# Kernel optimization log

Hardware: AMD Instinct MI355X
Metric: run time of the kernel (lower is better)

## Reference

```python
import jax, jax.numpy as jnp
import numpy as np

N_NODES, N_EDGES = 50000, 800000
IN, HID, HEADS, OUT = 128, 64, 4, 64


def _segment_softmax(e, seg, n):
    # softmax over edges grouped by source node (torch.sparse.softmax dim=1), per head
    m = jax.ops.segment_max(e, seg, num_segments=n)
    ex = jnp.exp(e - m[seg])
    s = jax.ops.segment_sum(ex, seg, num_segments=n)
    return ex / s[seg]


def _attention_layer(x, src, dst, lw, lb, aw, ab, final):
    n = x.shape[0]
    h = jax.nn.leaky_relu(x @ lw.T + lb, 0.2)            # (N, F)
    f = h.shape[1]
    # Faithful decomposition of Conv1d(2*F*H, H, k=1, groups=H) applied to
    # concat([tile(h_i, H), tile(h_j, H)]): group k covers tiled copies 2k and 2k+1;
    # copies < H come from h_i (src), copies >= H from h_j (dst).
    k = jnp.arange(HEADS)
    sel1 = (2 * k < HEADS).astype(h.dtype)[:, None]       # first half of group weights
    sel2 = (2 * k + 1 < HEADS).astype(h.dtype)[:, None]   # second half
    Wi = aw[:, :f] * sel1 + aw[:, f:] * sel2              # (H, F) acting on h_src
    Wj = aw[:, :f] * (1.0 - sel1) + aw[:, f:] * (1.0 - sel2)  # (H, F) acting on h_dst
    e = (h @ Wi.T)[src] + (h @ Wj.T)[dst] + ab            # (E, H)
    alpha = _segment_softmax(e, src, n)                   # (E, H)
    # h2[i] = sum_{j in N(i)} h[j] outer alpha[ij]  -> (N, F, H)
    h2 = jax.ops.segment_sum(h[dst][:, :, None] * alpha[:, None, :], src, num_segments=n)
    if final:
        return jax.nn.relu(h2.mean(axis=-1))              # (N, OUT)
    return jax.nn.relu(h2.reshape(n, -1))                 # (N, F*H)


def setup_inputs() -> dict:
    key = jax.random.key(0)
    ks = jax.random.split(key, 16)
    d = {}
    d["x"] = jax.random.normal(ks[0], (N_NODES, IN), jnp.float32)
    dims_in = [IN, HID * HEADS, HID * HEADS]
    dims_out = [HID, HID, OUT]
    i = 1
    for L in range(3):
        di, do = dims_in[L], dims_out[L]
        d[f"lin{L}_w"] = jax.random.normal(ks[i], (do, di), jnp.float32) / np.float32(np.sqrt(di)); i += 1
        d[f"lin{L}_b"] = jax.random.normal(ks[i], (do,), jnp.float32) * 0.01; i += 1
        d[f"att{L}_w"] = jax.random.normal(ks[i], (HEADS, 2 * do), jnp.float32) / np.float32(np.sqrt(2 * do)); i += 1
        d[f"att{L}_b"] = jax.random.normal(ks[i], (HEADS,), jnp.float32) * 0.01; i += 1
    d["src"] = jnp.sort(jax.random.randint(ks[13], (N_EDGES,), 0, N_NODES, dtype=jnp.int32))
    d["dst"] = jax.random.randint(ks[14], (N_EDGES,), 0, N_NODES, dtype=jnp.int32)
    return d


def reference(x, lin0_w, lin0_b, att0_w, att0_b, lin1_w, lin1_b, att1_w, att1_b,
              lin2_w, lin2_b, att2_w, att2_b, src, dst):
    layers = [(lin0_w, lin0_b, att0_w, att0_b),
              (lin1_w, lin1_b, att1_w, att1_b),
              (lin2_w, lin2_b, att2_w, att2_b)]
    out = x
    for i, (lw, lb, aw, ab) in enumerate(layers):
        out = _attention_layer(out, src, dst, lw, lb, aw, ab, final=(i == len(layers) - 1))
    return out
```

## Files before the change

kernel.cpp:

```cpp
#include <hip/hip_runtime.h>
#include <hip/hip_fp16.h>

#define N_NODES 50000
#define N_EDGES 800000
#define BUCKET_SPLIT 25000

typedef _Float16 half8 __attribute__((ext_vector_type(8)));
typedef _Float16 f16x4 __attribute__((ext_vector_type(4)));
typedef float floatx4 __attribute__((ext_vector_type(4)));

__global__ __launch_bounds__(256) void setup_kernel(const int* __restrict__ src,
                                                    const int* __restrict__ dst,
                                                    int* __restrict__ row_ptr,
                                                    int* __restrict__ row_mid,
                                                    int* __restrict__ dstp,
                                                    const float* __restrict__ lw0,
                                                    const float* __restrict__ lw1,
                                                    const float* __restrict__ lw2,
                                                    _Float16* __restrict__ w0p,
                                                    _Float16* __restrict__ w1p,
                                                    _Float16* __restrict__ w2p) {
    const int gid = blockIdx.x * 256 + threadIdx.x;
    const int gstride = gridDim.x * 256;
    for (int idx = gid; idx <= N_NODES; idx += gstride) {
        int lo = 0, hi = N_EDGES;
        while (lo < hi) {
            int mid = (lo + hi) >> 1;
            if (src[mid] < idx) lo = mid + 1; else hi = mid;
        }
        row_ptr[idx] = lo;
    }
    for (int i = gid; i < N_NODES; i += gstride) {
        int lo = 0, hi = N_EDGES;
        while (lo < hi) { int m = (lo + hi) >> 1; if (src[m] < i) lo = m + 1; else hi = m; }
        int lo1 = lo, hi1 = N_EDGES;
        while (lo1 < hi1) { int m = (lo1 + hi1) >> 1; if (src[m] < i + 1) lo1 = m + 1; else hi1 = m; }
        int c = lo;
        for (int e = lo; e < lo1; ++e) { int d = dst[e]; if (d < BUCKET_SPLIT) dstp[c++] = d; }
        row_mid[i] = c;
        for (int e = lo; e < lo1; ++e) { int d = dst[e]; if (d >= BUCKET_SPLIT) dstp[c++] = d; }
    }
    for (int idx = gid; idx < 64 * 128; idx += gstride) w0p[idx] = (_Float16)lw0[idx];
    for (int idx = gid; idx < 64 * 192; idx += gstride) {
        int o = idx / 192, r = idx % 192;
        int ch = r >> 6, f = r & 63;
        float v1, v2;
        if (ch == 0) {
            v1 = lw1[o * 256 + f * 4 + 0] + lw1[o * 256 + f * 4 + 1];
            v2 = lw2[o * 256 + f * 4 + 0] + lw2[o * 256 + f * 4 + 1];
        } else if (ch == 1) {
            v1 = lw1[o * 256 + f * 4 + 2];
            v2 = lw2[o * 256 + f * 4 + 2];
        } else {
            v1 = lw1[o * 256 + f * 4 + 3];
            v2 = lw2[o * 256 + f * 4 + 3];
        }
        w1p[idx] = (_Float16)v1;
        w2p[idx] = (_Float16)v2;
    }
}

template <typename TIn, int K>
__global__ __launch_bounds__(256) void lin_kernel(const TIn* __restrict__ in,
                                                  const _Float16* __restrict__ w,
                                                  const float* __restrict__ b,
                                                  const float* __restrict__ aw,
                                                  _Float16* __restrict__ h,
                                                  float2* __restrict__ s, int n) {
    const int t = threadIdx.x;
    const int l = t & 63;
    const int wv = t >> 6;
    const int arow = l & 15;
    const int kg = l >> 4;
    const long rowbase = (long)blockIdx.x * 64 + wv * 16;
    long arow_g = rowbase + arow;
    if (arow_g >= n) arow_g = n - 1;

    floatx4 acc[4] = {};

    for (int kc = 0; kc < K; kc += 32) {
        const int ks = kc + kg * 8;
        half8 a;
        if (sizeof(TIn) == 4) {
            const TIn* ap = in + arow_g * K + ks;
            #pragma unroll
            for (int j = 0; j < 8; ++j) a[j] = (_Float16)ap[j];
        } else {
            a = *(const half8*)((const _Float16*)in + arow_g * K + ks);
        }
        #pragma unroll
        for (int ct = 0; ct < 4; ++ct) {
            half8 bb = *(const half8*)(w + (long)(ct * 16 + arow) * K + ks);
            acc[ct] = __builtin_amdgcn_mfma_f32_16x16x32_f16(a, bb, acc[ct], 0, 0, 0);
        }
    }

    const int c = l & 15;
    const int rq = l >> 4;
    float bias[4], a2c[4], a3c[4];
    #pragma unroll
    for (int ct = 0; ct < 4; ++ct) {
        int col = ct * 16 + c;
        bias[ct] = b[col];
        a2c[ct] = aw[2 * 128 + col] + aw[2 * 128 + 64 + col];
        a3c[ct] = aw[3 * 128 + col] + aw[3 * 128 + 64 + col];
    }
    #pragma unroll
    for (int r = 0; r < 4; ++r) {
        long row = rowbase + rq * 4 + r;
        bool ok = row < n;
        float q2 = 0.f, q3 = 0.f;
        _Float16 hv[4];
        #pragma unroll
        for (int ct = 0; ct < 4; ++ct) {
            float u = acc[ct][r] + bias[ct];
            u = u > 0.f ? u : 0.2f * u;
            q2 += u * a2c[ct];
            q3 += u * a3c[ct];
            hv[ct] = (_Float16)u;
        }
        if (ok) {
            #pragma unroll
            for (int ct = 0; ct < 4; ++ct) h[row * 64 + ct * 16 + c] = hv[ct];
        }
        #pragma unroll
        for (int o = 1; o < 16; o <<= 1) {
            q2 += __shfl_xor(q2, o);
            q3 += __shfl_xor(q3, o);
        }
        if (c == 0 && ok) s[row] = make_float2(__expf(q2), __expf(q3));
    }
}

template <int FINAL>
__global__ __launch_bounds__(256) void layer_kernel(const _Float16* __restrict__ hfeat,
                                                    const float2* __restrict__ E,
                                                    const int* __restrict__ dstp,
                                                    const int* __restrict__ row_ptr,
                                                    const int* __restrict__ row_mid,
                                                    const _Float16* __restrict__ w,
                                                    const float* __restrict__ b,
                                                    const float* __restrict__ aw,
                                                    _Float16* __restrict__ h_out,
                                                    float2* __restrict__ s_out,
                                                    float* __restrict__ out_f) {
    __shared__ _Float16 g_lds[16][200];
    __shared__ float2 spart[4][16];

    const int t = threadIdx.x;
    const int l = t & 63;
    const int wv = t >> 6;
    const int q = l >> 4;
    const int fl = l & 15;
    const int base = blockIdx.x * 16;
    const int i = base + wv * 4 + q;

    const int r0 = row_ptr[i], r1 = row_ptr[i + 1], rm = row_mid[i];
    const int deg = r1 - r0;

    float am[4] = {}, a2[4] = {}, a3[4] = {};
    float S2 = 0.f, S3 = 0.f;

    #pragma unroll
    for (int pp = 0; pp < 2; ++pp) {
        const int p = pp ^ (int)(blockIdx.x & 1);
        const int plo = p ? rm : r0;
        const int phi = p ? r1 : rm;
        const int pdeg = phi - plo;
        int md = pdeg;
        md = max(md, __shfl_xor(md, 16));
        md = max(md, __shfl_xor(md, 32));
        const int psafe = pdeg > 0 ? phi - 1 : 0;

        for (int c0 = 0; c0 < md; c0 += 16) {
            const int dl = dstp[min(plo + c0 + fl, psafe)];
            const int jn = min(16, md - c0);
            for (int j = 0; j < jn; j += 4) {
                int dg[4]; float vm[4];
                #pragma unroll
                for (int g = 0; g < 4; ++g) {
                    const int sl = j + g;
                    dg[g] = __shfl(dl, (q << 4) | sl);
                    vm[g] = (c0 + sl < pdeg) ? 1.f : 0.f;
                }
                f16x4 hv[4]; float2 Ev[4];
                #pragma unroll
                for (int g = 0; g < 4; ++g) {
                    hv[g] = *(const f16x4*)(hfeat + (long)dg[g] * 64 + fl * 4);
                    Ev[g] = E[dg[g]];
                }
                #pragma unroll
                for (int g = 0; g < 4; ++g) {
                    const float e2 = vm[g] * Ev[g].x, e3 = vm[g] * Ev[g].y;
                    S2 += e2; S3 += e3;
                    #pragma unroll
                    for (int k = 0; k < 4; ++k) {
                        const float hf = (float)hv[g][k];
                        am[k] += vm[g] * hf;
                        a2[k] += e2 * hf;
                        a3[k] += e3 * hf;
                    }
                }
            }
        }
    }

    const float inv_deg = deg > 0 ? 1.f / (float)deg : 0.f;
    const float i2 = deg > 0 ? 1.f / S2 : 0.f;
    const float i3 = deg > 0 ? 1.f / S3 : 0.f;

    if (FINAL) {
        floatx4 o;
        #pragma unroll
        for (int k = 0; k < 4; ++k)
            o[k] = fmaxf(0.5f * inv_deg * am[k] + 0.25f * (a2[k] * i2 + a3[k] * i3), 0.f);
        *(floatx4*)(out_f + (long)i * 64 + fl * 4) = o;
        return;
    }

    {
        const int nl = wv * 4 + q;
        f16x4 o0, o1, o2;
        #pragma unroll
        for (int k = 0; k < 4; ++k) {
            o0[k] = (_Float16)fmaxf(am[k] * inv_deg, 0.f);
            o1[k] = (_Float16)fmaxf(a2[k] * i2, 0.f);
            o2[k] = (_Float16)fmaxf(a3[k] * i3, 0.f);
        }
        *(f16x4*)(&g_lds[nl][fl * 4])       = o0;
        *(f16x4*)(&g_lds[nl][64 + fl * 4])  = o1;
        *(f16x4*)(&g_lds[nl][128 + fl * 4]) = o2;
    }
    __syncthreads();

    floatx4 acc = {};
    #pragma unroll
    for (int kc = 0; kc < 192; kc += 32) {
        const int ks = kc + q * 8;
        half8 a = *(const half8*)(&g_lds[fl][ks]);
        half8 bb = *(const half8*)(w + (long)(wv * 16 + fl) * 192 + ks);
        acc = __builtin_amdgcn_mfma_f32_16x16x32_f16(a, bb, acc, 0, 0, 0);
    }

    const int col = wv * 16 + fl;
    const float bias = b[col];
    const float a2c = aw[2 * 128 + col] + aw[2 * 128 + 64 + col];
    const float a3c = aw[3 * 128 + col] + aw[3 * 128 + 64 + col];
    #pragma unroll
    for (int r = 0; r < 4; ++r) {
        const int row = q * 4 + r;
        float u = acc[r] + bias;
        u = u > 0.f ? u : 0.2f * u;
        h_out[(long)(base + row) * 64 + col] = (_Float16)u;
        float q2 = u * a2c, q3 = u * a3c;
        #pragma unroll
        for (int o = 1; o < 16; o <<= 1) {
            q2 += __shfl_xor(q2, o);
            q3 += __shfl_xor(q3, o);
        }
        if (fl == 0) spart[wv][row] = make_float2(q2, q3);
    }
    __syncthreads();
    if (t < 16) {
        const float2 p0 = spart[0][t], p1 = spart[1][t], p2 = spart[2][t], p3 = spart[3][t];
        s_out[base + t] = make_float2(__expf(p0.x + p1.x + p2.x + p3.x),
                                      __expf(p0.y + p1.y + p2.y + p3.y));
    }
}

extern "C" void kernel_launch(void* const* d_in, const int* in_sizes, int n_in,
                              void* d_out, int out_size, void* d_ws, size_t ws_size,
                              hipStream_t stream) {
    const float* x = (const float*)d_in[0];
    const float* lw0 = (const float*)d_in[1];
    const float* lb0 = (const float*)d_in[2];
    const float* aw0 = (const float*)d_in[3];
    const float* lw1 = (const float*)d_in[5];
    const float* lb1 = (const float*)d_in[6];
    const float* aw1 = (const float*)d_in[7];
    const float* lw2 = (const float*)d_in[9];
    const float* lb2 = (const float*)d_in[10];
    const float* aw2 = (const float*)d_in[11];
    const int* src = (const int*)d_in[13];
    const int* dst = (const int*)d_in[14];
    float* out = (float*)d_out;

    const int N = N_NODES;

    _Float16* hA = (_Float16*)d_ws;
    _Float16* hB = hA + (size_t)N * 64;
    float2* sA = (float2*)(hB + (size_t)N * 64);
    float2* sB = sA + N;
    _Float16* w0p = (_Float16*)(sB + N);
    _Float16* w1p = w0p + 64 * 128;
    _Float16* w2p = w1p + 64 * 192;
    int* row_ptr = (int*)(w2p + 64 * 192);
    int* row_mid = row_ptr + N + 1;
    int* dstp = row_mid + N;

    const int lin_grid = (N + 63) / 64;
    const int layer_grid = N / 16;

    setup_kernel<<<196, 256, 0, stream>>>(src, dst, row_ptr, row_mid, dstp,
                                          lw0, lw1, lw2, w0p, w1p, w2p);
    lin_kernel<float, 128><<<lin_grid, 256, 0, stream>>>(x, w0p, lb0, aw0, hA, sA, N);
    layer_kernel<0><<<layer_grid, 256, 0, stream>>>(hA, sA, dstp, row_ptr, row_mid,
                                                    w1p, lb1, aw1, hB, sB, out);
    layer_kernel<0><<<layer_grid, 256, 0, stream>>>(hB, sB, dstp, row_ptr, row_mid,
                                                    w2p, lb2, aw2, hA, sA, out);
    layer_kernel<1><<<layer_grid, 256, 0, stream>>>(hA, sA, dstp, row_ptr, row_mid,
                                                    w2p, lb2, aw2, hB, sB, out);
}
```

Before: 233.1 us.

## Sort nodes by degree to balance gather work, drop destination bucket split

```diff
diff --git a/kernel.cpp b/kernel.cpp
--- a/kernel.cpp
+++ b/kernel.cpp
@@ -3,17 +3,14 @@
 
 #define N_NODES 50000
 #define N_EDGES 800000
-#define BUCKET_SPLIT 25000
 
 typedef _Float16 half8 __attribute__((ext_vector_type(8)));
 typedef _Float16 f16x4 __attribute__((ext_vector_type(4)));
 typedef float floatx4 __attribute__((ext_vector_type(4)));
 
 __global__ __launch_bounds__(256) void setup_kernel(const int* __restrict__ src,
-                                                    const int* __restrict__ dst,
                                                     int* __restrict__ row_ptr,
-                                                    int* __restrict__ row_mid,
-                                                    int* __restrict__ dstp,
+                                                    int* __restrict__ bins,
                                                     const float* __restrict__ lw0,
                                                     const float* __restrict__ lw1,
                                                     const float* __restrict__ lw2,
@@ -35,10 +32,8 @@
         while (lo < hi) { int m = (lo + hi) >> 1; if (src[m] < i) lo = m + 1; else hi = m; }
         int lo1 = lo, hi1 = N_EDGES;
         while (lo1 < hi1) { int m = (lo1 + hi1) >> 1; if (src[m] < i + 1) lo1 = m + 1; else hi1 = m; }
-        int c = lo;
-        for (int e = lo; e < lo1; ++e) { int d = dst[e]; if (d < BUCKET_SPLIT) dstp[c++] = d; }
-        row_mid[i] = c;
-        for (int e = lo; e < lo1; ++e) { int d = dst[e]; if (d >= BUCKET_SPLIT) dstp[c++] = d; }
+        int deg = lo1 - lo;
+        atomicAdd(&bins[deg < 127 ? deg : 127], 1);
     }
     for (int idx = gid; idx < 64 * 128; idx += gstride) w0p[idx] = (_Float16)lw0[idx];
     for (int idx = gid; idx < 64 * 192; idx += gstride) {
@@ -57,6 +52,33 @@
         }
         w1p[idx] = (_Float16)v1;
         w2p[idx] = (_Float16)v2;
+    }
+}
+
+__global__ __launch_bounds__(128) void scan_kernel(int* __restrict__ bins) {
+    __shared__ int tmp[128];
+    const int t = threadIdx.x;
+    const int cnt = bins[127 - t];
+    tmp[t] = cnt;
+    __syncthreads();
+    for (int o = 1; o < 128; o <<= 1) {
+        int u = (t >= o) ? tmp[t - o] : 0;
+        __syncthreads();
+        tmp[t] += u;
+        __syncthreads();
+    }
+    bins[127 - t] = tmp[t] - cnt;
+}
+
+__global__ __launch_bounds__(256) void scatter_kernel(const int* __restrict__ row_ptr,
+                                                      int* __restrict__ bins,
+                                                      int* __restrict__ order) {
+    const int gid = blockIdx.x * 256 + threadIdx.x;
+    const int gstride = gridDim.x * 256;
+    for (int i = gid; i < N_NODES; i += gstride) {
+        int deg = row_ptr[i + 1] - row_ptr[i];
+        int pos = atomicAdd(&bins[deg < 127 ? deg : 127], 1);
+        order[pos] = i;
     }
 }
 
@@ -135,9 +157,9 @@
 template <int FINAL>
 __global__ __launch_bounds__(256) void layer_kernel(const _Float16* __restrict__ hfeat,
                                                     const float2* __restrict__ E,
-                                                    const int* __restrict__ dstp,
+                                                    const int* __restrict__ dst,
                                                     const int* __restrict__ row_ptr,
-                                                    const int* __restrict__ row_mid,
+                                                    const int* __restrict__ order,
                                                     const _Float16* __restrict__ w,
                                                     const float* __restrict__ b,
                                                     const float* __restrict__ aw,
@@ -146,6 +168,7 @@
                                                     float* __restrict__ out_f) {
     __shared__ _Float16 g_lds[16][200];
     __shared__ float2 spart[4][16];
+    __shared__ int ordt[16];
 
     const int t = threadIdx.x;
     const int l = t & 63;
@@ -153,53 +176,49 @@
     const int q = l >> 4;
     const int fl = l & 15;
     const int base = blockIdx.x * 16;
-    const int i = base + wv * 4 + q;
-
-    const int r0 = row_ptr[i], r1 = row_ptr[i + 1], rm = row_mid[i];
-    const int deg = r1 - r0;
+
+    if (t < 16) ordt[t] = order[base + t];
+    __syncthreads();
+
+    const int i = ordt[wv * 4 + q];
+
+    const int r0 = row_ptr[i];
+    const int deg = row_ptr[i + 1] - r0;
+    int md = deg;
+    md = max(md, __shfl_xor(md, 16));
+    md = max(md, __shfl_xor(md, 32));
 
     float am[4] = {}, a2[4] = {}, a3[4] = {};
     float S2 = 0.f, S3 = 0.f;
-
-    #pragma unroll
-    for (int pp = 0; pp < 2; ++pp) {
-        const int p = pp ^ (int)(blockIdx.x & 1);
-        const int plo = p ? rm : r0;
-        const int phi = p ? r1 : rm;
-        const int pdeg = phi - plo;
-        int md = pdeg;
-        md = max(md, __shfl_xor(md, 16));
-        md = max(md, __shfl_xor(md, 32));
-        const int psafe = pdeg > 0 ? phi - 1 : 0;
-
-        for (int c0 = 0; c0 < md; c0 += 16) {
-            const int dl = dstp[min(plo + c0 + fl, psafe)];
-            const int jn = min(16, md - c0);
-            for (int j = 0; j < jn; j += 4) {
-                int dg[4]; float vm[4];
+    const int safew = deg > 0 ? r0 + deg - 1 : 0;
+
+    for (int c0 = 0; c0 < md; c0 += 16) {
+        const int dl = dst[min(r0 + c0 + fl, safew)];
+        const int jn = min(16, md - c0);
+        for (int j = 0; j < jn; j += 4) {
+            int dg[4]; float vm[4];
+            #pragma unroll
+            for (int g = 0; g < 4; ++g) {
+                const int sl = j + g;
+                dg[g] = __shfl(dl, (q << 4) | sl);
+                vm[g] = (c0 + sl < deg) ? 1.f : 0.f;
+            }
+            f16x4 hv[4]; float2 Ev[4];
+            #pragma unroll
+            for (int g = 0; g < 4; ++g) {
+                hv[g] = *(const f16x4*)(hfeat + (long)dg[g] * 64 + fl * 4);
+                Ev[g] = E[dg[g]];
+            }
+            #pragma unroll
+            for (int g = 0; g < 4; ++g) {
+                const float e2 = vm[g] * Ev[g].x, e3 = vm[g] * Ev[g].y;
+                S2 += e2; S3 += e3;
                 #pragma unroll
-                for (int g = 0; g < 4; ++g) {
-                    const int sl = j + g;
-                    dg[g] = __shfl(dl, (q << 4) | sl);
-                    vm[g] = (c0 + sl < pdeg) ? 1.f : 0.f;
-                }
-                f16x4 hv[4]; float2 Ev[4];
-                #pragma unroll
-                for (int g = 0; g < 4; ++g) {
-                    hv[g] = *(const f16x4*)(hfeat + (long)dg[g] * 64 + fl * 4);
-                    Ev[g] = E[dg[g]];
-                }
-                #pragma unroll
-                for (int g = 0; g < 4; ++g) {
-                    const float e2 = vm[g] * Ev[g].x, e3 = vm[g] * Ev[g].y;
-                    S2 += e2; S3 += e3;
-                    #pragma unroll
-                    for (int k = 0; k < 4; ++k) {
-                        const float hf = (float)hv[g][k];
-                        am[k] += vm[g] * hf;
-                        a2[k] += e2 * hf;
-                        a3[k] += e3 * hf;
-                    }
+                for (int k = 0; k < 4; ++k) {
+                    const float hf = (float)hv[g][k];
+                    am[k] += vm[g] * hf;
+                    a2[k] += e2 * hf;
+                    a3[k] += e3 * hf;
                 }
             }
         }
@@ -251,7 +270,7 @@
         const int row = q * 4 + r;
         float u = acc[r] + bias;
         u = u > 0.f ? u : 0.2f * u;
-        h_out[(long)(base + row) * 64 + col] = (_Float16)u;
+        h_out[(long)ordt[row] * 64 + col] = (_Float16)u;
         float q2 = u * a2c, q3 = u * a3c;
         #pragma unroll
         for (int o = 1; o < 16; o <<= 1) {
@@ -263,8 +282,8 @@
     __syncthreads();
     if (t < 16) {
         const float2 p0 = spart[0][t], p1 = spart[1][t], p2 = spart[2][t], p3 = spart[3][t];
-        s_out[base + t] = make_float2(__expf(p0.x + p1.x + p2.x + p3.x),
-                                      __expf(p0.y + p1.y + p2.y + p3.y));
+        s_out[ordt[t]] = make_float2(__expf(p0.x + p1.x + p2.x + p3.x),
+                                     __expf(p0.y + p1.y + p2.y + p3.y));
     }
 }
 
@@ -295,19 +314,22 @@
     _Float16* w1p = w0p + 64 * 128;
     _Float16* w2p = w1p + 64 * 192;
     int* row_ptr = (int*)(w2p + 64 * 192);
-    int* row_mid = row_ptr + N + 1;
-    int* dstp = row_mid + N;
+    int* bins = row_ptr + N + 1;
+    int* order = bins + 128;
 
     const int lin_grid = (N + 63) / 64;
     const int layer_grid = N / 16;
 
-    setup_kernel<<<196, 256, 0, stream>>>(src, dst, row_ptr, row_mid, dstp,
-                                          lw0, lw1, lw2, w0p, w1p, w2p);
+    hipMemsetAsync(bins, 0, 128 * sizeof(int), stream);
+    setup_kernel<<<196, 256, 0, stream>>>(src, row_ptr, bins, lw0, lw1, lw2,
+                                          w0p, w1p, w2p);
+    scan_kernel<<<1, 128, 0, stream>>>(bins);
+    scatter_kernel<<<196, 256, 0, stream>>>(row_ptr, bins, order);
     lin_kernel<float, 128><<<lin_grid, 256, 0, stream>>>(x, w0p, lb0, aw0, hA, sA, N);
-    layer_kernel<0><<<layer_grid, 256, 0, stream>>>(hA, sA, dstp, row_ptr, row_mid,
+    layer_kernel<0><<<layer_grid, 256, 0, stream>>>(hA, sA, dst, row_ptr, order,
                                                     w1p, lb1, aw1, hB, sB, out);
-    layer_kernel<0><<<layer_grid, 256, 0, stream>>>(hB, sB, dstp, row_ptr, row_mid,
+    layer_kernel<0><<<layer_grid, 256, 0, stream>>>(hB, sB, dst, row_ptr, order,
                                                     w2p, lb2, aw2, hA, sA, out);
-    layer_kernel<1><<<layer_grid, 256, 0, stream>>>(hA, sA, dstp, row_ptr, row_mid,
+    layer_kernel<1><<<layer_grid, 256, 0, stream>>>(hA, sA, dst, row_ptr, order,
                                                     w2p, lb2, aw2, hB, sB, out);
 }
```

Result: slower. 443.9 us (+90.5%).

## Drop dst bucket split and software-pipeline neighbor gathers in layer kernel

Applied to the files above, without the earlier changes.

```diff
diff --git a/kernel.cpp b/kernel.cpp
--- a/kernel.cpp
+++ b/kernel.cpp
@@ -3,17 +3,13 @@
 
 #define N_NODES 50000
 #define N_EDGES 800000
-#define BUCKET_SPLIT 25000
 
 typedef _Float16 half8 __attribute__((ext_vector_type(8)));
 typedef _Float16 f16x4 __attribute__((ext_vector_type(4)));
 typedef float floatx4 __attribute__((ext_vector_type(4)));
 
 __global__ __launch_bounds__(256) void setup_kernel(const int* __restrict__ src,
-                                                    const int* __restrict__ dst,
                                                     int* __restrict__ row_ptr,
-                                                    int* __restrict__ row_mid,
-                                                    int* __restrict__ dstp,
                                                     const float* __restrict__ lw0,
                                                     const float* __restrict__ lw1,
                                                     const float* __restrict__ lw2,
@@ -29,16 +25,6 @@
             if (src[mid] < idx) lo = mid + 1; else hi = mid;
         }
         row_ptr[idx] = lo;
-    }
-    for (int i = gid; i < N_NODES; i += gstride) {
-        int lo = 0, hi = N_EDGES;
-        while (lo < hi) { int m = (lo + hi) >> 1; if (src[m] < i) lo = m + 1; else hi = m; }
-        int lo1 = lo, hi1 = N_EDGES;
-        while (lo1 < hi1) { int m = (lo1 + hi1) >> 1; if (src[m] < i + 1) lo1 = m + 1; else hi1 = m; }
-        int c = lo;
-        for (int e = lo; e < lo1; ++e) { int d = dst[e]; if (d < BUCKET_SPLIT) dstp[c++] = d; }
-        row_mid[i] = c;
-        for (int e = lo; e < lo1; ++e) { int d = dst[e]; if (d >= BUCKET_SPLIT) dstp[c++] = d; }
     }
     for (int idx = gid; idx < 64 * 128; idx += gstride) w0p[idx] = (_Float16)lw0[idx];
     for (int idx = gid; idx < 64 * 192; idx += gstride) {
@@ -132,12 +118,42 @@
     }
 }
 
+#define LOADB(DG, VM, HV, EV, JBASE)                                        \
+    {                                                                       \
+        _Pragma("unroll")                                                   \
+        for (int g = 0; g < 4; ++g) {                                       \
+            const int sl = (JBASE) + g;                   \
+            DG[g] = __shfl(dl, (q << 4) | sl);                              \
+            VM[g] = (c0 + sl < deg) ? 1.f : 0.f;                            \
+        }                                                                   \
+        _Pragma("unroll")                                                   \
+        for (int g = 0; g < 4; ++g) {                                       \
+            HV[g] = *(const f16x4*)(hfeat + (long)DG[g] * 64 + fl * 4);     \
+            EV[g] = E[DG[g]];                                               \
+        }                                                                   \
+    }
+
+#define CONSB(VM, HV, EV)                                                   \
+    {                                                                       \
+        _Pragma("unroll")                                                   \
+        for (int g = 0; g < 4; ++g) {                                       \
+            const float e2 = VM[g] * EV[g].x, e3 = VM[g] * EV[g].y;         \
+            S2 += e2; S3 += e3;                                             \
+            _Pragma("unroll")                                               \
+            for (int k = 0; k < 4; ++k) {                                   \
+                const float hf = (float)HV[g][k];                           \
+                am[k] += VM[g] * hf;                                        \
+                a2[k] += e2 * hf;                                           \
+                a3[k] += e3 * hf;                                           \
+            }                                                               \
+        }                                                                   \
+    }
+
 template <int FINAL>
 __global__ __launch_bounds__(256) void layer_kernel(const _Float16* __restrict__ hfeat,
                                                     const float2* __restrict__ E,
-                                                    const int* __restrict__ dstp,
+                                                    const int* __restrict__ dst,
                                                     const int* __restrict__ row_ptr,
-                                                    const int* __restrict__ row_mid,
                                                     const _Float16* __restrict__ w,
                                                     const float* __restrict__ b,
                                                     const float* __restrict__ aw,
@@ -155,53 +171,39 @@
     const int base = blockIdx.x * 16;
     const int i = base + wv * 4 + q;
 
-    const int r0 = row_ptr[i], r1 = row_ptr[i + 1], rm = row_mid[i];
-    const int deg = r1 - r0;
+    const int r0 = row_ptr[i];
+    const int deg = row_ptr[i + 1] - r0;
+    int md = deg;
+    md = max(md, __shfl_xor(md, 16));
+    md = max(md, __shfl_xor(md, 32));
 
     float am[4] = {}, a2[4] = {}, a3[4] = {};
     float S2 = 0.f, S3 = 0.f;
-
-    #pragma unroll
-    for (int pp = 0; pp < 2; ++pp) {
-        const int p = pp ^ (int)(blockIdx.x & 1);
-        const int plo = p ? rm : r0;
-        const int phi = p ? r1 : rm;
-        const int pdeg = phi - plo;
-        int md = pdeg;
-        md = max(md, __shfl_xor(md, 16));
-        md = max(md, __shfl_xor(md, 32));
-        const int psafe = pdeg > 0 ? phi - 1 : 0;
-
+    const int safew = deg > 0 ? r0 + deg - 1 : 0;
+
+    if (md > 0) {
+        int dl = dst[min(r0 + fl, safew)];
         for (int c0 = 0; c0 < md; c0 += 16) {
-            const int dl = dstp[min(plo + c0 + fl, psafe)];
+            const int hasnext = (c0 + 16 < md);
+            const int dln = hasnext ? dst[min(r0 + c0 + 16 + fl, safew)] : 0;
             const int jn = min(16, md - c0);
-            for (int j = 0; j < jn; j += 4) {
-                int dg[4]; float vm[4];
-                #pragma unroll
-                for (int g = 0; g < 4; ++g) {
-                    const int sl = j + g;
-                    dg[g] = __shfl(dl, (q << 4) | sl);
-                    vm[g] = (c0 + sl < pdeg) ? 1.f : 0.f;
-                }
-                f16x4 hv[4]; float2 Ev[4];
-                #pragma unroll
-                for (int g = 0; g < 4; ++g) {
-                    hv[g] = *(const f16x4*)(hfeat + (long)dg[g] * 64 + fl * 4);
-                    Ev[g] = E[dg[g]];
-                }
-                #pragma unroll
-                for (int g = 0; g < 4; ++g) {
-                    const float e2 = vm[g] * Ev[g].x, e3 = vm[g] * Ev[g].y;
-                    S2 += e2; S3 += e3;
-                    #pragma unroll
-                    for (int k = 0; k < 4; ++k) {
-                        const float hf = (float)hv[g][k];
-                        am[k] += vm[g] * hf;
-                        a2[k] += e2 * hf;
-                        a3[k] += e3 * hf;
-                    }
-                }
+
+            int dgA[4], dgB[4];
+            float vmA[4], vmB[4];
+            f16x4 hvA[4], hvB[4];
+            float2 EvA[4], EvB[4];
+
+            LOADB(dgA, vmA, hvA, EvA, 0);
+            int j = 0;
+            while (true) {
+                if (j + 4 < jn) LOADB(dgB, vmB, hvB, EvB, j + 4);
+                CONSB(vmA, hvA, EvA);
+                j += 4; if (j >= jn) break;
+                if (j + 4 < jn) LOADB(dgA, vmA, hvA, EvA, j + 4);
+                CONSB(vmB, hvB, EvB);
+                j += 4; if (j >= jn) break;
             }
+            dl = dln;
         }
     }
 
@@ -295,19 +297,17 @@
     _Float16* w1p = w0p + 64 * 128;
     _Float16* w2p = w1p + 64 * 192;
     int* row_ptr = (int*)(w2p + 64 * 192);
-    int* row_mid = row_ptr + N + 1;
-    int* dstp = row_mid + N;
 
     const int lin_grid = (N + 63) / 64;
     const int layer_grid = N / 16;
 
-    setup_kernel<<<196, 256, 0, stream>>>(src, dst, row_ptr, row_mid, dstp,
-                                          lw0, lw1, lw2, w0p, w1p, w2p);
+    setup_kernel<<<196, 256, 0, stream>>>(src, row_ptr, lw0, lw1, lw2,
+                                          w0p, w1p, w2p);
     lin_kernel<float, 128><<<lin_grid, 256, 0, stream>>>(x, w0p, lb0, aw0, hA, sA, N);
-    layer_kernel<0><<<layer_grid, 256, 0, stream>>>(hA, sA, dstp, row_ptr, row_mid,
+    layer_kernel<0><<<layer_grid, 256, 0, stream>>>(hA, sA, dst, row_ptr,
                                                     w1p, lb1, aw1, hB, sB, out);
-    layer_kernel<0><<<layer_grid, 256, 0, stream>>>(hB, sB, dstp, row_ptr, row_mid,
+    layer_kernel<0><<<layer_grid, 256, 0, stream>>>(hB, sB, dst, row_ptr,
                                                     w2p, lb2, aw2, hA, sA, out);
-    layer_kernel<1><<<layer_grid, 256, 0, stream>>>(hA, sA, dstp, row_ptr, row_mid,
+    layer_kernel<1><<<layer_grid, 256, 0, stream>>>(hA, sA, dst, row_ptr,
                                                     w2p, lb2, aw2, hB, sB, out);
 }
```

Result: faster. 213.9 us (-8.2%).
